# Kernel optimization log

Measured on AMD Instinct MI355X. Metric: run time of the kernel, lower is better.

The kernel has to match this reference:

```python
import jax, jax.numpy as jnp
import numpy as np
from jax.nn import gelu

L = 4        # N_layers
M = 32       # N_modes
PA = 48      # n_processor_a
PB = 48      # n_processor_b
P = PA + PB
IN_A, IN_B = 3, 3
OUT_A, OUT_B = 1, 1
HA, HB = 256, 128
K = 3        # kernel_size
S3 = 0.05


def setup_inputs() -> dict:
    key = jax.random.key(0)
    ks = jax.random.split(key, 24)
    n = lambda k, shp, s=1.0: jax.random.normal(k, shp, dtype=jnp.float32) * s
    w_sc = 0.1
    inp = {
        "u_a": n(ks[0], (1, HA, HA)),
        "x_a": n(ks[1], (2, HA, HA)),
        "u_b": n(ks[2], (1, HB, HB)),
        "x_b": n(ks[3], (2, HB, HB)),
        # 1x1 convs stored as (Cout, Cin) matrices (equinox stores (Cout,Cin,1,1); same math)
        "enc_a_w": n(ks[4], (PA, IN_A), w_sc), "enc_a_b": n(ks[5], (PA,), w_sc),
        "enc_b_w": n(ks[6], (PB, IN_B), w_sc), "enc_b_b": n(ks[7], (PB,), w_sc),
        "dec_a_w": n(ks[8], (OUT_A, PA), w_sc), "dec_a_b": n(ks[9], (OUT_A,), w_sc),
        "dec_b_w": n(ks[10], (OUT_B, PB), w_sc), "dec_b_b": n(ks[11], (OUT_B,), w_sc),
        "c1a_w": n(ks[12], (L, PA, PA), w_sc), "c1a_b": n(ks[13], (L, PA), w_sc),
        "c2a_w": n(ks[14], (L, PA, PA), w_sc), "c2a_b": n(ks[15], (L, PA), w_sc),
        "c1b_w": n(ks[16], (L, PB, PB, K, K), w_sc), "c1b_b": n(ks[17], (L, PB), w_sc),
        "c2b_w": n(ks[18], (L, PB, PB, K, K), w_sc), "c2b_b": n(ks[19], (L, PB), w_sc),
        # complex spectral weights A as real/imag float32 parts
        "A_re": n(ks[20], (L, P, P, M, M), S3),
        "A_im": n(ks[21], (L, P, P, M, M), S3),
    }
    return inp


def _conv1x1(x, w, b):
    # x: (Cin, H, W), w: (Cout, Cin)
    return jnp.einsum("oi,ihw->ohw", w, x) + b[:, None, None]


def _convk(x, w, b):
    # x: (Cin, H, W), w: (Cout, Cin, K, K), SAME padding (padding = K//2)
    y = jax.lax.conv_general_dilated(x[None], w, (1, 1), "SAME",
                                     dimension_numbers=("NCHW", "OIHW", "NCHW"))[0]
    return y + b[:, None, None]


def _rfft2_truncate(x, m):
    c = jnp.fft.rfft2(x, norm="forward")[:, :, :m]
    return jnp.roll(c, m // 2, axis=1)[:, :m]


def _irfft2_pad(c, m, s):
    c = jnp.pad(c, ((0, 0), (0, s[0] - c.shape[1]), (0, s[1] - c.shape[2])))
    c = jnp.roll(c, -m // 2, axis=1)
    return jnp.fft.irfft2(c, s=s, norm="forward")


def _spectral(ua, ub, W):
    m = W.shape[2]
    coeff = jnp.concatenate([_rfft2_truncate(ua, m), _rfft2_truncate(ub, m)], axis=0)  # (P, m, m)
    coeff = jnp.einsum("pqmn,qmn->pmn", W, coeff)
    oa = _irfft2_pad(coeff[: ua.shape[0]], m, ua.shape[1:])
    ob = _irfft2_pad(coeff[ua.shape[0]:], m, ub.shape[1:])
    return oa, ob


def reference(u_a, x_a, u_b, x_b,
              enc_a_w, enc_a_b, enc_b_w, enc_b_b,
              dec_a_w, dec_a_b, dec_b_w, dec_b_b,
              c1a_w, c1a_b, c2a_w, c2a_b,
              c1b_w, c1b_b, c2b_w, c2b_b,
              A_re, A_im):
    ua = _conv1x1(jnp.concatenate([x_a, u_a], 0), enc_a_w, enc_a_b)
    ub = _conv1x1(jnp.concatenate([x_b, u_b], 0), enc_b_w, enc_b_b)
    for i in range(A_re.shape[0]):
        Wi = (A_re[i] + 1j * A_im[i]).astype(jnp.complex64)
        ua_, ub_ = _spectral(ua, ub, Wi)
        ua = ua + gelu(_conv1x1(gelu(_conv1x1(ua_, c1a_w[i], c1a_b[i])), c2a_w[i], c2a_b[i]))
        ub = ub + gelu(_convk(gelu(_convk(ub_, c1b_w[i], c1b_b[i])), c2b_w[i], c2b_b[i]))
    out_a = _conv1x1(ua, dec_a_w, dec_a_b)
    out_b = _conv1x1(ub, dec_b_w, dec_b_b)
    return (out_a, out_b)
```

## Files before the change

kernel.cpp:

```cpp
#include <hip/hip_runtime.h>

#define HA 256
#define WA 256
#define HB 128
#define WB 128
#define PA 48
#define PB 48
#define PP 96
#define MM 32
#define NPIXA (HA*WA)
#define NPIXB (HB*WB)

typedef short bf16x8 __attribute__((ext_vector_type(8)));
typedef float f32x4 __attribute__((ext_vector_type(4)));

__device__ __forceinline__ float gelu_f(float x) {
    float z = 0.7978845608028654f * (x + 0.044715f * x * x * x);
    float e = __expf(2.0f * z);
    return x - x / (e + 1.0f);
}

__device__ __forceinline__ short f2bf(float f) {
    unsigned u = __float_as_uint(f);
    unsigned r = (u + 0x7FFFu + ((u >> 16) & 1u)) >> 16;
    return (short)r;
}

__device__ __forceinline__ unsigned pack2(float a, float b) {
    return (unsigned)(unsigned short)f2bf(a) | ((unsigned)(unsigned short)f2bf(b) << 16);
}

__global__ __launch_bounds__(256) void k_pre(
        float* tiyA, float* tixB, float* tiyB, short* T2x,
        const float* u_a, const float* x_a, const float* u_b, const float* x_b,
        const float* wa, const float* ba, const float* wb, const float* bb,
        float* UA, float* UB,
        const float* c1b_w, const float* c2b_w, short* WT,
        short* TbfA, short* TbfB,
        const float* c1a_w, const float* c2a_w, short* WcT,
        short* Ty2A, short* Ty2B,
        short* TyIA, short* TyIB, short* T2xB) {
    const float TWO_PI = 6.28318530717958647692f;
    int bid = blockIdx.x;
    if (bid < 48) {
        int t = bid * 256 + threadIdx.x;
        if (t < MM * WA) {
            int k = t / WA, x = t - k * WA;
            int m = (k * x) & (WA - 1);
            float ang = TWO_PI * (float)m / (float)WA;
            float s, c; __sincosf(ang, &s, &c);
            float wgt = (k == 0) ? 1.0f : 2.0f;
            T2x[x*64 + 2*k]   = f2bf(wgt * c);
            T2x[x*64 + 2*k+1] = f2bf(-wgt * s);
            int ky = k - 16;
            int my = (ky * x) & (HA - 1);
            float angy = TWO_PI * (float)my / (float)HA;
            float sy, cy; __sincosf(angy, &sy, &cy);
            tiyA[2*t] = cy; tiyA[2*t+1] = sy;
        } else if (t < MM * WA + MM * WB) {
            int t2 = t - MM * WA;
            int k = t2 / WB, x = t2 - k * WB;
            int m = (k * x) & (WB - 1);
            float ang = TWO_PI * (float)m / (float)WB;
            float s, c; __sincosf(ang, &s, &c);
            float wgt = (k == 0) ? 1.0f : 2.0f;
            tixB[2*t2] = wgt * c; tixB[2*t2+1] = wgt * s;
            int ky = k - 16;
            int my = (ky * x) & (HB - 1);
            float angy = TWO_PI * (float)my / (float)HB;
            float sy, cy; __sincosf(angy, &sy, &cy);
            tiyB[2*t2] = cy; tiyB[2*t2+1] = sy;
        }
    } else if (bid < 15408) {
        int eb = bid - 48;
        int o = eb / 320;
        int chunk = eb - o * 320;
        if (chunk < 256) {
            int pix = chunk * 256 + threadIdx.x;
            UA[(size_t)o*NPIXA + pix] = wa[o*3+0]*x_a[pix] + wa[o*3+1]*x_a[NPIXA+pix]
                                      + wa[o*3+2]*u_a[pix] + ba[o];
        } else {
            int pix = (chunk - 256) * 256 + threadIdx.x;
            UB[(size_t)o*NPIXB + pix] = wb[o*3+0]*x_b[pix] + wb[o*3+1]*x_b[NPIXB+pix]
                                      + wb[o*3+2]*u_b[pix] + bb[o];
        }
    } else if (bid < 16272) {
        int g = (bid - 15408) * 256 + threadIdx.x;
        if (g < 4*2*9*48*64) {
            int l  = g / 55296;
            int r1 = g - l*55296;
            int cv = r1 / 27648;
            int r2 = r1 - cv*27648;
            int tap = r2 / 3072;
            int r3 = r2 - tap*3072;
            int oc = r3 >> 6;
            int ic = r3 & 63;
            const float* src = cv ? c2b_w : c1b_w;
            float v = 0.f;
            if (ic < 48) v = src[(((size_t)l*48 + oc)*48 + ic)*9 + tap];
            WT[g] = f2bf(v);
        }
    } else if (bid < 16336) {
        int g = (bid - 16272) * 256 + threadIdx.x;
        int col = g >> 8, x = g & 255;
        int k = col >> 1, comp = col & 1;
        int m = (k * x) & (WA - 1);
        float ang = TWO_PI * (float)m / (float)WA;
        float s, c; __sincosf(ang, &s, &c);
        float sc = 1.0f / (float)(HA * WA);
        TbfA[col*WA + x] = f2bf(comp ? -s * sc : c * sc);
    } else if (bid < 16368) {
        int g = (bid - 16336) * 256 + threadIdx.x;
        int col = g >> 7, x = g & 127;
        int k = col >> 1, comp = col & 1;
        int m = (k * x) & (WB - 1);
        float ang = TWO_PI * (float)m / (float)WB;
        float s, c; __sincosf(ang, &s, &c);
        float sc = 1.0f / (float)(HB * WB);
        TbfB[col*WB + x] = f2bf(comp ? -s * sc : c * sc);
    } else if (bid < 16464) {
        int g = (bid - 16368) * 256 + threadIdx.x;
        int l  = g / 6144;
        int r  = g - l*6144;
        int cv = r / 3072;
        int r2 = r - cv*3072;
        int oc = r2 >> 6;
        int ic = r2 & 63;
        const float* src = cv ? c2a_w : c1a_w;
        float v = 0.f;
        if (ic < 48) v = src[((size_t)l*48 + oc)*48 + ic];
        WcT[g] = f2bf(v);
    } else if (bid < 16592) {
        int g = (bid - 16464) * 256 + threadIdx.x;
        int row = g >> 9, col = g & 511;
        int j = row >> 1, comp = row & 1;
        int y = col >> 1, comp2 = col & 1;
        int my = ((j - 16) * y) & (HA - 1);
        float ang = TWO_PI * (float)my / (float)HA;
        float sy, cy; __sincosf(ang, &sy, &cy);
        float v = comp == 0 ? (comp2 == 0 ? cy : sy) : (comp2 == 0 ? -sy : cy);
        Ty2A[g] = f2bf(v);
    } else if (bid < 16656) {
        int g = (bid - 16592) * 256 + threadIdx.x;
        int row = g >> 8, col = g & 255;
        int j = row >> 1, comp = row & 1;
        int y = col >> 1, comp2 = col & 1;
        int my = ((j - 16) * y) & (HB - 1);
        float ang = TWO_PI * (float)my / (float)HB;
        float sy, cy; __sincosf(ang, &sy, &cy);
        float v = comp == 0 ? (comp2 == 0 ? cy : sy) : (comp2 == 0 ? -sy : cy);
        Ty2B[g] = f2bf(v);
    } else if (bid < 16720) {
        int g = (bid - 16656) * 256 + threadIdx.x;
        int y = g >> 6, col = g & 63;
        int j = col >> 1, comp = col & 1;
        int my = ((j - 16) * y) & (HA - 1);
        float ang = TWO_PI * (float)my / (float)HA;
        float sy, cy; __sincosf(ang, &sy, &cy);
        TyIA[g] = f2bf(comp ? sy : cy);
    } else if (bid < 16752) {
        int g = (bid - 16720) * 256 + threadIdx.x;
        int y = g >> 6, col = g & 63;
        int j = col >> 1, comp = col & 1;
        int my = ((j - 16) * y) & (HB - 1);
        float ang = TWO_PI * (float)my / (float)HB;
        float sy, cy; __sincosf(ang, &sy, &cy);
        TyIB[g] = f2bf(comp ? sy : cy);
    } else {
        int g = (bid - 16752) * 256 + threadIdx.x;
        int x = g >> 6, col = g & 63;
        int k = col >> 1, comp = col & 1;
        int m = (k * x) & (WB - 1);
        float ang = TWO_PI * (float)m / (float)WB;
        float s, c; __sincosf(ang, &s, &c);
        float wgt = (k == 0) ? 1.0f : 2.0f;
        T2xB[g] = f2bf(comp ? -wgt * s : wgt * c);
    }
}

__global__ __launch_bounds__(256) void k_fwd_x(
        const float* __restrict__ UA, const float* __restrict__ UB,
        short* __restrict__ FTA, short* __restrict__ FTB,
        const short* __restrict__ TbfA, const short* __restrict__ TbfB) {
    extern __shared__ short lsb[];
    int bid = blockIdx.x;
    const float* U; short* FT; const short* T; int N, ymask, cshift;
    if (bid < 384) { U = UA; FT = FTA; T = TbfA; N = WA; ymask = 255; cshift = 8; }
    else { bid -= 384; U = UB; FT = FTB; T = TbfB; N = WB; ymask = 127; cshift = 7; }
    int r0 = bid * 32;
    int c = r0 >> cshift;
    int ybase = r0 & ymask;
    int NP = N + 8;
    int nq = N >> 2;
    const float4* src = (const float4*)(U + (size_t)r0 * N);
    for (int i = threadIdx.x; i < 32*nq; i += 256) {
        int r = i / nq, q = i - r*nq;
        float4 v = src[i];
        *(uint2*)(lsb + r*NP + q*4) = make_uint2(pack2(v.x, v.y), pack2(v.z, v.w));
    }
    __syncthreads();
    int wv = threadIdx.x >> 6, lane = threadIdx.x & 63;
    int n = lane & 15, kg = lane >> 4;
    int col = wv*16 + n;
    const short* Tc = T + (size_t)col * N;
    f32x4 acc0 = {0.f,0.f,0.f,0.f}, acc1 = {0.f,0.f,0.f,0.f};
    for (int ks = 0; ks < (N >> 5); ++ks) {
        bf16x8 bfrag = *(const bf16x8*)(Tc + ks*32 + kg*8);
        bf16x8 a0 = *(const bf16x8*)(lsb + (size_t)n*NP + ks*32 + kg*8);
        bf16x8 a1 = *(const bf16x8*)(lsb + (size_t)(16+n)*NP + ks*32 + kg*8);
        acc0 = __builtin_amdgcn_mfma_f32_16x16x32_bf16(a0, bfrag, acc0, 0, 0, 0);
        acc1 = __builtin_amdgcn_mfma_f32_16x16x32_bf16(a1, bfrag, acc1, 0, 0, 0);
    }
    __syncthreads();
    short* trb = lsb;
    #pragma unroll
    for (int r = 0; r < 4; ++r) {
        trb[col*36 + kg*4 + r]      = f2bf(acc0[r]);
        trb[col*36 + 16 + kg*4 + r] = f2bf(acc1[r]);
    }
    __syncthreads();
    int K2 = 2 * (ymask + 1);
    for (int idx = threadIdx.x; idx < 512; idx += 256) {
        int kx = idx >> 4, q = idx & 15;
        int yl = q * 2;
        unsigned lo = (unsigned)(unsigned short)trb[(2*kx+0)*36 + yl]
                    | ((unsigned)(unsigned short)trb[(2*kx+1)*36 + yl] << 16);
        unsigned hi = (unsigned)(unsigned short)trb[(2*kx+0)*36 + yl+1]
                    | ((unsigned)(unsigned short)trb[(2*kx+1)*36 + yl+1] << 16);
        *(uint2*)(FT + ((size_t)(c*32 + kx))*K2 + 2*(size_t)ybase + yl*2) = make_uint2(lo, hi);
    }
}

__global__ __launch_bounds__(256) void k_fwd_y(
        const short* __restrict__ FTA, const short* __restrict__ FTB,
        const short* __restrict__ Ty2A, const short* __restrict__ Ty2B,
        float* __restrict__ CINa, float* __restrict__ CINb) {
    __shared__ short lsb[32*264];
    int bid = blockIdx.x;
    const short* FT; const short* Ty; int K2, NP, pbase, c, h;
    if (bid < 96) { c = bid>>1; h = bid&1; FT = FTA; Ty = Ty2A; K2 = 512; NP = 264; pbase = 0; }
    else { int b2 = bid - 96; c = b2>>1; h = b2&1; FT = FTB; Ty = Ty2B; K2 = 256; NP = 136; pbase = 48; }
    float* CO = (h == 0) ? CINa : CINb;
    int hlen = K2 >> 1;
    int nchunk = hlen >> 3;
    for (int idx = threadIdx.x; idx < 32*nchunk; idx += 256) {
        int row = idx / nchunk, q = idx - row*nchunk;
        *(uint4*)(lsb + row*NP + q*8) =
            *(const uint4*)(FT + ((size_t)c*32 + row)*K2 + h*hlen + q*8);
    }
    __syncthreads();
    int w = threadIdx.x >> 6, lane = threadIdx.x & 63;
    int n = lane & 15, kg = lane >> 4;
    f32x4 acc0 = {0.f,0.f,0.f,0.f}, acc1 = {0.f,0.f,0.f,0.f};
    int nks = hlen >> 5;
    for (int ks = 0; ks < nks; ++ks) {
        bf16x8 af = *(const bf16x8*)(Ty + (size_t)(w*16 + n)*K2 + h*hlen + ks*32 + kg*8);
        bf16x8 b0 = *(const bf16x8*)(lsb + n*NP + ks*32 + kg*8);
        bf16x8 b1 = *(const bf16x8*)(lsb + (16+n)*NP + ks*32 + kg*8);
        acc0 = __builtin_amdgcn_mfma_f32_16x16x32_bf16(af, b0, acc0, 0, 0, 0);
        acc1 = __builtin_amdgcn_mfma_f32_16x16x32_bf16(af, b1, acc1, 0, 0, 0);
    }
    #pragma unroll
    for (int r = 0; r < 4; ++r) {
        int row = w*16 + kg*4 + r;
        int j = row >> 1, comp = row & 1;
        size_t base = (((size_t)(pbase + c))*32 + j)*32;
        CO[(base + n)*2 + comp]      = acc0[r];
        CO[(base + 16 + n)*2 + comp] = acc1[r];
    }
}

__global__ __launch_bounds__(256) void k_spectral(
        const float* __restrict__ Wre, const float* __restrict__ Wim,
        const float* __restrict__ CINa, const float* __restrict__ CINb,
        float2* __restrict__ PART) {
    int part = blockIdx.y;
    int t = blockIdx.x * 256 + threadIdx.x;
    int p = t >> 8;
    int m4 = (t & 255) << 2;
    int q0 = part * 12;
    const float4* wr = (const float4*)(Wre + ((size_t)p * PP + q0) * 1024 + m4);
    const float4* wi = (const float4*)(Wim + ((size_t)p * PP + q0) * 1024 + m4);
    const float4* ca = (const float4*)(CINa + (size_t)q0 * 2048 + m4*2);
    const float4* cb = (const float4*)(CINb + (size_t)q0 * 2048 + m4*2);
    float re0=0,re1=0,re2=0,re3=0, im0=0,im1=0,im2=0,im3=0;
    #pragma unroll
    for (int q = 0; q < 12; ++q) {
        float4 a = wr[q * 256];
        float4 b = wi[q * 256];
        float4 c0 = ca[q * 512];
        float4 c1 = ca[q * 512 + 1];
        float4 d0 = cb[q * 512];
        float4 d1 = cb[q * 512 + 1];
        float cr0 = c0.x + d0.x, ci0 = c0.y + d0.y;
        float cr1 = c0.z + d0.z, ci1 = c0.w + d0.w;
        float cr2 = c1.x + d1.x, ci2 = c1.y + d1.y;
        float cr3 = c1.z + d1.z, ci3 = c1.w + d1.w;
        re0 += a.x*cr0 - b.x*ci0;  im0 += a.x*ci0 + b.x*cr0;
        re1 += a.y*cr1 - b.y*ci1;  im1 += a.y*ci1 + b.y*cr1;
        re2 += a.z*cr2 - b.z*ci2;  im2 += a.z*ci2 + b.z*cr2;
        re3 += a.w*cr3 - b.w*ci3;  im3 += a.w*ci3 + b.w*cr3;
    }
    float2* po = PART + ((size_t)part * PP + p) * 1024 + m4;
    po[0] = make_float2(re0, im0);
    po[1] = make_float2(re1, im1);
    po[2] = make_float2(re2, im2);
    po[3] = make_float2(re3, im3);
}

__global__ __launch_bounds__(256) void k_invy(
        const float2* __restrict__ PART,
        const short* __restrict__ TyIA, const short* __restrict__ TyIB,
        short* __restrict__ DA, short* __restrict__ DB) {
    __shared__ short A2[64*72];
    int bid = blockIdx.x;
    int c, yh, cb; const short* Ty; short* D;
    if (bid < 96) { c = bid >> 1; yh = bid & 1; Ty = TyIA; D = DA; cb = c; }
    else { c = bid - 96 + 48; yh = 0; Ty = TyIB; D = DB; cb = c - 48; }
    for (int idx = threadIdx.x; idx < 1024; idx += 256) {
        int j = idx >> 5, kx = idx & 31;
        float re = 0.f, im = 0.f;
        const float2* pp = PART + (size_t)c*1024 + idx;
        #pragma unroll
        for (int u = 0; u < 8; ++u) {
            float2 v = pp[(size_t)u*PP*1024];
            re += v.x; im += v.y;
        }
        A2[(2*kx+0)*72 + 2*j]   = f2bf(re);
        A2[(2*kx+0)*72 + 2*j+1] = f2bf(-im);
        A2[(2*kx+1)*72 + 2*j]   = f2bf(im);
        A2[(2*kx+1)*72 + 2*j+1] = f2bf(re);
    }
    __syncthreads();
    int wv = threadIdx.x >> 6, lane = threadIdx.x & 63;
    int n = lane & 15, kg = lane >> 4;
    #pragma unroll
    for (int ntl = 0; ntl < 2; ++ntl) {
        int nt = wv*2 + ntl;
        int y = yh*128 + nt*16 + n;
        bf16x8 bf0 = *(const bf16x8*)(Ty + (size_t)y*64 + kg*8);
        bf16x8 bf1 = *(const bf16x8*)(Ty + (size_t)y*64 + 32 + kg*8);
        #pragma unroll
        for (int mt = 0; mt < 4; ++mt) {
            bf16x8 a0 = *(const bf16x8*)(A2 + (mt*16 + n)*72 + kg*8);
            bf16x8 a1 = *(const bf16x8*)(A2 + (mt*16 + n)*72 + 32 + kg*8);
            f32x4 acc = {0.f,0.f,0.f,0.f};
            acc = __builtin_amdgcn_mfma_f32_16x16x32_bf16(a0, bf0, acc, 0, 0, 0);
            acc = __builtin_amdgcn_mfma_f32_16x16x32_bf16(a1, bf1, acc, 0, 0, 0);
            int row0 = mt*16 + kg*4;
            *(uint2*)(D + (size_t)y*3072 + cb*64 + row0) =
                make_uint2(pack2(acc[0], acc[1]), pack2(acc[2], acc[3]));
        }
    }
}

__global__ __launch_bounds__(256) void k_inv(
        const short* __restrict__ DA, const short* __restrict__ DB,
        float* __restrict__ UA, short* __restrict__ SBbf,
        const short* __restrict__ T2x, const short* __restrict__ T2xB,
        const short* __restrict__ W1T, const short* __restrict__ W2T,
        const float* __restrict__ b1v, const float* __restrict__ b2v) {
    __shared__ __attribute__((aligned(16))) char smc[37888];
    int t = threadIdx.x;
    int wv = t >> 6, lane = t & 63;
    int n = lane & 15, kg = lane >> 4;
    if (blockIdx.x < 512) {
        short* b0bf  = (short*)smc;
        short* slbf  = (short*)(smc + 18432);
        float* bl1   = (float*)(smc + 37120);
        float* bl2   = (float*)(smc + 37312);
        int y  = blockIdx.x >> 1;
        int xh = (blockIdx.x & 1) << 7;
        if (t >= 64 && t < 112) bl1[t-64] = b1v[t-64];
        if (t >= 128 && t < 176) bl2[t-128] = b2v[t-128];
        const short* DAy = DA + (size_t)y*3072;
        {
            f32x4 acc[2][3];
            #pragma unroll
            for (int i = 0; i < 2; ++i)
                #pragma unroll
                for (int mt = 0; mt < 3; ++mt)
                    acc[i][mt] = (f32x4){0.f,0.f,0.f,0.f};
            #pragma unroll
            for (int ks = 0; ks < 2; ++ks) {
                bf16x8 bfr[2];
                #pragma unroll
                for (int i = 0; i < 2; ++i) {
                    int px = xh + (wv*2 + i)*16 + n;
                    bfr[i] = *(const bf16x8*)(T2x + (size_t)px*64 + ks*32 + kg*8);
                }
                #pragma unroll
                for (int mt = 0; mt < 3; ++mt) {
                    bf16x8 af = *(const bf16x8*)(DAy + (mt*16 + n)*64 + ks*32 + kg*8);
                    #pragma unroll
                    for (int i = 0; i < 2; ++i)
                        acc[i][mt] = __builtin_amdgcn_mfma_f32_16x16x32_bf16(af, bfr[i], acc[i][mt], 0, 0, 0);
                }
            }
            #pragma unroll
            for (int i = 0; i < 2; ++i) {
                int xl = (wv*2 + i)*16 + n;
                #pragma unroll
                for (int mt = 0; mt < 3; ++mt)
                    #pragma unroll
                    for (int r = 0; r < 4; ++r)
                        slbf[xl*72 + mt*16 + kg*4 + r] = f2bf(acc[i][mt][r]);
            }
            for (int idx = t; idx < 2048; idx += 256)
                slbf[(idx >> 4)*72 + 48 + (idx & 15)] = 0;
        }
        __syncthreads();
        {
            bf16x8 aw[3][2];
            #pragma unroll
            for (int mt = 0; mt < 3; ++mt)
                #pragma unroll
                for (int ks = 0; ks < 2; ++ks)
                    aw[mt][ks] = *(const bf16x8*)(W1T + (size_t)(mt*16 + n)*64 + ks*32 + kg*8);
            f32x4 acc[2][3];
            #pragma unroll
            for (int nt = 0; nt < 2; ++nt)
                #pragma unroll
                for (int mt = 0; mt < 3; ++mt)
                    acc[nt][mt] = (f32x4){0.f,0.f,0.f,0.f};
            #pragma unroll
            for (int nt = 0; nt < 2; ++nt) {
                int ntile = wv*2 + nt;
                #pragma unroll
                for (int ks = 0; ks < 2; ++ks) {
                    bf16x8 bfrag = *(const bf16x8*)(slbf + (size_t)(ntile*16 + n)*72 + ks*32 + kg*8);
                    #pragma unroll
                    for (int mt = 0; mt < 3; ++mt)
                        acc[nt][mt] = __builtin_amdgcn_mfma_f32_16x16x32_bf16(aw[mt][ks], bfrag, acc[nt][mt], 0, 0, 0);
                }
            }
            #pragma unroll
            for (int nt = 0; nt < 2; ++nt) {
                int px = (wv*2 + nt)*16 + n;
                #pragma unroll
                for (int mt = 0; mt < 3; ++mt) {
                    int oc0 = mt*16 + kg*4;
                    float g0 = gelu_f(acc[nt][mt][0] + bl1[oc0+0]);
                    float g1 = gelu_f(acc[nt][mt][1] + bl1[oc0+1]);
                    float g2 = gelu_f(acc[nt][mt][2] + bl1[oc0+2]);
                    float g3 = gelu_f(acc[nt][mt][3] + bl1[oc0+3]);
                    *(uint2*)(b0bf + (size_t)px*72 + oc0) = make_uint2(pack2(g0,g1), pack2(g2,g3));
                }
            }
            for (int idx = t; idx < 2048; idx += 256)
                b0bf[(idx >> 4)*72 + 48 + (idx & 15)] = 0;
        }
        __syncthreads();
        {
            bf16x8 aw[3][2];
            #pragma unroll
            for (int mt = 0; mt < 3; ++mt)
                #pragma unroll
                for (int ks = 0; ks < 2; ++ks)
                    aw[mt][ks] = *(const bf16x8*)(W2T + (size_t)(mt*16 + n)*64 + ks*32 + kg*8);
            f32x4 acc[2][3];
            #pragma unroll
            for (int nt = 0; nt < 2; ++nt)
                #pragma unroll
                for (int mt = 0; mt < 3; ++mt)
                    acc[nt][mt] = (f32x4){0.f,0.f,0.f,0.f};
            #pragma unroll
            for (int nt = 0; nt < 2; ++nt) {
                int ntile = wv*2 + nt;
                #pragma unroll
                for (int ks = 0; ks < 2; ++ks) {
                    bf16x8 bfrag = *(const bf16x8*)(b0bf + (size_t)(ntile*16 + n)*72 + ks*32 + kg*8);
                    #pragma unroll
                    for (int mt = 0; mt < 3; ++mt)
                        acc[nt][mt] = __builtin_amdgcn_mfma_f32_16x16x32_bf16(aw[mt][ks], bfrag, acc[nt][mt], 0, 0, 0);
                }
            }
            #pragma unroll
            for (int nt = 0; nt < 2; ++nt) {
                int px = (wv*2 + nt)*16 + n;
                #pragma unroll
                for (int mt = 0; mt < 3; ++mt) {
                    int oc0 = mt*16 + kg*4;
                    #pragma unroll
                    for (int r = 0; r < 4; ++r) {
                        int oc = oc0 + r;
                        size_t o = (size_t)oc*NPIXA + (size_t)y*WA + xh + px;
                        UA[o] = gelu_f(acc[nt][mt][r] + bl2[oc]) + UA[o];
                    }
                }
            }
        }
    } else {
        int y = blockIdx.x - 512;
        short* sbuf = (short*)smc;
        const short* DBy = DB + (size_t)y*3072;
        #pragma unroll
        for (int ntl = 0; ntl < 2; ++ntl) {
            int nt = wv*2 + ntl;
            int x = nt*16 + n;
            bf16x8 bf0 = *(const bf16x8*)(T2xB + (size_t)x*64 + kg*8);
            bf16x8 bf1 = *(const bf16x8*)(T2xB + (size_t)x*64 + 32 + kg*8);
            #pragma unroll
            for (int mt = 0; mt < 3; ++mt) {
                bf16x8 a0 = *(const bf16x8*)(DBy + (mt*16 + n)*64 + kg*8);
                bf16x8 a1 = *(const bf16x8*)(DBy + (mt*16 + n)*64 + 32 + kg*8);
                f32x4 acc = {0.f,0.f,0.f,0.f};
                acc = __builtin_amdgcn_mfma_f32_16x16x32_bf16(a0, bf0, acc, 0, 0, 0);
                acc = __builtin_amdgcn_mfma_f32_16x16x32_bf16(a1, bf1, acc, 0, 0, 0);
                int c0 = mt*16 + kg*4;
                #pragma unroll
                for (int r = 0; r < 4; ++r)
                    sbuf[(c0 + r)*132 + x] = f2bf(acc[r]);
            }
        }
        __syncthreads();
        for (int idx = t; idx < 3072; idx += 256) {
            int x = idx / 24, cu = idx - x*24;
            unsigned v = (unsigned)(unsigned short)sbuf[(2*cu)*132 + x]
                       | ((unsigned)(unsigned short)sbuf[(2*cu+1)*132 + x] << 16);
            *(unsigned*)(SBbf + ((size_t)y*WB + x)*48 + 2*cu) = v;
        }
    }
}

__global__ __launch_bounds__(384) void k_conv3x3_mfma(
        const short* __restrict__ in, float* __restrict__ outf,
        short* __restrict__ outbf,
        const short* __restrict__ wt, const float* __restrict__ bias,
        const float* resid) {
    __shared__ __attribute__((aligned(16))) short tile[3*34*72];
    int y  = blockIdx.x >> 2;
    int x0 = (blockIdx.x & 3) << 5;
    int tid = threadIdx.x;
    for (int idx = tid; idx < 102*6; idx += 384) {
        int pix = idx / 6, chunk = idx - pix*6;
        int r = pix / 34, px = pix - r*34;
        int gy = y - 1 + r, gx = x0 - 1 + px;
        uint4 v = {0u,0u,0u,0u};
        if (gy >= 0 && gy < HB && gx >= 0 && gx < WB)
            v = *(const uint4*)(in + ((size_t)gy*WB + gx)*48 + chunk*8);
        *(uint4*)(tile + pix*72 + chunk*8) = v;
    }
    for (int idx = tid; idx < 102*2; idx += 384) {
        int pix = idx >> 1, h = idx & 1;
        *(uint4*)(tile + pix*72 + 48 + h*8) = (uint4){0u,0u,0u,0u};
    }
    __syncthreads();

    int wv = tid / 64, lane = tid & 63;
    int n = lane & 15, kg = lane >> 4;
    int nt = wv & 1, mt = wv >> 1;
    f32x4 acc = {0.f,0.f,0.f,0.f};
    #pragma unroll
    for (int tap = 0; tap < 9; ++tap) {
        int dy = tap / 3, dx = tap - dy*3;
        int pxl = nt*16 + n + dx;
        const short* brow = tile + (dy*34 + pxl)*72;
        const short* ap = wt + (size_t)tap*3072 + (size_t)(mt*16 + n)*64;
        #pragma unroll
        for (int ks = 0; ks < 2; ++ks) {
            bf16x8 bfrag = *(const bf16x8*)(brow + ks*32 + kg*8);
            bf16x8 afrag = *(const bf16x8*)(ap + ks*32 + kg*8);
            acc = __builtin_amdgcn_mfma_f32_16x16x32_bf16(afrag, bfrag, acc, 0, 0, 0);
        }
    }
    int px_g = x0 + nt*16 + n;
    int oc0 = mt*16 + kg*4;
    float g0 = gelu_f(acc[0] + bias[oc0+0]);
    float g1 = gelu_f(acc[1] + bias[oc0+1]);
    float g2 = gelu_f(acc[2] + bias[oc0+2]);
    float g3 = gelu_f(acc[3] + bias[oc0+3]);
    if (outbf) {
        *(uint2*)(outbf + ((size_t)y*WB + px_g)*48 + oc0) =
            make_uint2(pack2(g0, g1), pack2(g2, g3));
    } else {
        float gv[4] = {g0, g1, g2, g3};
        #pragma unroll
        for (int r = 0; r < 4; ++r) {
            size_t o = (size_t)(oc0 + r)*NPIXB + (size_t)y*WB + px_g;
            outf[o] = gv[r] + resid[o];
        }
    }
}

__global__ __launch_bounds__(256) void k_decode(
        const float* __restrict__ UA, const float* __restrict__ UB,
        const float* dwa, const float* dba,
        const float* dwb, const float* dbb, float* outp) {
    int t = blockIdx.x*256 + threadIdx.x;
    if (t < NPIXA) {
        float acc = dba[0];
        #pragma unroll 8
        for (int p = 0; p < PA; ++p) acc += dwa[p]*UA[(size_t)p*NPIXA + t];
        outp[t] = acc;
    } else {
        int u = t - NPIXA;
        float acc = dbb[0];
        #pragma unroll 8
        for (int p = 0; p < PB; ++p) acc += dwb[p]*UB[(size_t)p*NPIXB + u];
        outp[t] = acc;
    }
}

extern "C" void kernel_launch(void* const* d_in, const int* in_sizes, int n_in,
                              void* d_out, int out_size, void* d_ws, size_t ws_size,
                              hipStream_t stream) {
    const float* u_a   = (const float*)d_in[0];
    const float* x_a   = (const float*)d_in[1];
    const float* u_b   = (const float*)d_in[2];
    const float* x_b   = (const float*)d_in[3];
    const float* enc_a_w = (const float*)d_in[4];
    const float* enc_a_b = (const float*)d_in[5];
    const float* enc_b_w = (const float*)d_in[6];
    const float* enc_b_b = (const float*)d_in[7];
    const float* dec_a_w = (const float*)d_in[8];
    const float* dec_a_b = (const float*)d_in[9];
    const float* dec_b_w = (const float*)d_in[10];
    const float* dec_b_b = (const float*)d_in[11];
    const float* c1a_w = (const float*)d_in[12];
    const float* c1a_b = (const float*)d_in[13];
    const float* c2a_w = (const float*)d_in[14];
    const float* c2a_b = (const float*)d_in[15];
    const float* c1b_w = (const float*)d_in[16];
    const float* c1b_b = (const float*)d_in[17];
    const float* c2b_w = (const float*)d_in[18];
    const float* c2b_b = (const float*)d_in[19];
    const float* A_re = (const float*)d_in[20];
    const float* A_im = (const float*)d_in[21];

    float* ws = (float*)d_ws;
    size_t off = 0;
    auto alloc = [&](size_t n) { float* p = ws + off; off += n; return p; };
    short* WT    = (short*)alloc(4*2*9*48*64/2);
    short* TbfA  = (short*)alloc(64*WA/2);
    short* TbfB  = (short*)alloc(64*WB/2);
    short* WcT   = (short*)alloc(4*2*48*64/2);
    short* T2x   = (short*)alloc(WA*64/2);
    short* T2xB  = (short*)alloc(WB*64/2);
    short* Ty2A  = (short*)alloc(64*512/2);
    short* Ty2B  = (short*)alloc(64*256/2);
    short* TyIA  = (short*)alloc(HA*64/2);
    short* TyIB  = (short*)alloc(HB*64/2);
    float* TiyA  = alloc(MM*HA*2);
    float* TixB  = alloc(MM*WB*2);
    float* TiyB  = alloc(MM*HB*2);
    float* UA = alloc((size_t)PA*NPIXA);
    float* UB = alloc((size_t)PB*NPIXB);
    short* SBbf = (short*)alloc((size_t)PB*NPIXB/2);
    short* TBbf = (short*)alloc((size_t)PB*NPIXB/2);
    short* FTA = (short*)alloc((size_t)PA*MM*512/2);
    short* FTB = (short*)alloc((size_t)PB*MM*256/2);
    short* DA  = (short*)alloc((size_t)HA*3072/2);
    short* DB  = (short*)alloc((size_t)HB*3072/2);
    float* CINa = alloc((size_t)PP*MM*MM*2);
    float* CINb = alloc((size_t)PP*MM*MM*2);
    float2* PART = (float2*)alloc((size_t)8*PP*MM*MM*2);
    if (off * sizeof(float) > ws_size) return;

    k_pre<<<dim3(16784), dim3(256), 0, stream>>>(
        TiyA, TixB, TiyB, T2x,
        u_a,x_a,u_b,x_b, enc_a_w,enc_a_b,enc_b_w,enc_b_b, UA,UB,
        c1b_w, c2b_w, WT, TbfA, TbfB, c1a_w, c2a_w, WcT, Ty2A, Ty2B,
        TyIA, TyIB, T2xB);
    for (int l = 0; l < 4; ++l) {
        k_fwd_x<<<dim3(576), dim3(256), 32*(WA+8)*2, stream>>>(UA,UB,FTA,FTB,TbfA,TbfB);
        k_fwd_y<<<dim3(192), dim3(256), 0, stream>>>(FTA,FTB,Ty2A,Ty2B,CINa,CINb);
        k_spectral<<<dim3(96,8), dim3(256), 0, stream>>>(
            A_re + (size_t)l*PP*PP*MM*MM, A_im + (size_t)l*PP*PP*MM*MM,
            CINa, CINb, PART);
        k_invy<<<dim3(144), dim3(256), 0, stream>>>(PART, TyIA, TyIB, DA, DB);
        k_inv<<<dim3(512 + 128), dim3(256), 0, stream>>>(DA, DB, UA, SBbf,
            T2x, T2xB,
            WcT + (size_t)(l*2 + 0)*3072, WcT + (size_t)(l*2 + 1)*3072,
            c1a_b + (size_t)l*PA, c2a_b + (size_t)l*PA);
        k_conv3x3_mfma<<<dim3(512), dim3(384), 0, stream>>>(SBbf, (float*)nullptr, TBbf,
            WT + (size_t)(l*2 + 0)*27648, c1b_b + (size_t)l*PB, (const float*)nullptr);
        k_conv3x3_mfma<<<dim3(512), dim3(384), 0, stream>>>(TBbf, UB, (short*)nullptr,
            WT + (size_t)(l*2 + 1)*27648, c2b_b + (size_t)l*PB, UB);
    }
    k_decode<<<dim3(320), dim3(256), 0, stream>>>(UA, UB,
        dec_a_w, dec_a_b, dec_b_w, dec_b_b, (float*)d_out);
}
```

Baseline: 308.0 us.

## Split fwd_y K into quarters with reduction kernel; double invy and conv3x3 grids

The forward y-DFT kernel now splits its reduction dimension four ways instead of two, writing four partial coefficient buffers. A new small kernel sums them once, so the spectral kernel reads a single pre-summed input instead of adding two buffers in every block. The inverse-y kernel and the 3x3 convolution are also split into smaller blocks (twice as many, each doing half the work) to raise parallelism across CUs. The cost is one extra kernel launch per layer, more partial-sum traffic, and more halo reloads in the narrower conv tiles.

```diff
diff --git a/kernel.cpp b/kernel.cpp
--- a/kernel.cpp
+++ b/kernel.cpp
@@ -234,14 +234,14 @@
 __global__ __launch_bounds__(256) void k_fwd_y(
         const short* __restrict__ FTA, const short* __restrict__ FTB,
         const short* __restrict__ Ty2A, const short* __restrict__ Ty2B,
-        float* __restrict__ CINa, float* __restrict__ CINb) {
-    __shared__ short lsb[32*264];
+        float* __restrict__ CIN4) {
+    __shared__ short lsb[32*136];
     int bid = blockIdx.x;
     const short* FT; const short* Ty; int K2, NP, pbase, c, h;
-    if (bid < 96) { c = bid>>1; h = bid&1; FT = FTA; Ty = Ty2A; K2 = 512; NP = 264; pbase = 0; }
-    else { int b2 = bid - 96; c = b2>>1; h = b2&1; FT = FTB; Ty = Ty2B; K2 = 256; NP = 136; pbase = 48; }
-    float* CO = (h == 0) ? CINa : CINb;
-    int hlen = K2 >> 1;
+    if (bid < 192) { c = bid>>2; h = bid&3; FT = FTA; Ty = Ty2A; K2 = 512; NP = 136; pbase = 0; }
+    else { int b2 = bid - 192; c = b2>>2; h = b2&3; FT = FTB; Ty = Ty2B; K2 = 256; NP = 72; pbase = 48; }
+    float* CO = CIN4 + (size_t)h * (PP*MM*MM*2);
+    int hlen = K2 >> 2;
     int nchunk = hlen >> 3;
     for (int idx = threadIdx.x; idx < 32*nchunk; idx += 256) {
         int row = idx / nchunk, q = idx - row*nchunk;
@@ -270,10 +270,18 @@
     }
 }
 
+__global__ __launch_bounds__(256) void k_csum(
+        const float4* __restrict__ CIN4, float4* __restrict__ CINs) {
+    int t = blockIdx.x * 256 + threadIdx.x;
+    const int S = PP*MM*MM*2/4;
+    float4 a = CIN4[t], b = CIN4[t + S], c = CIN4[t + 2*S], d = CIN4[t + 3*S];
+    CINs[t] = make_float4(a.x+b.x+c.x+d.x, a.y+b.y+c.y+d.y,
+                          a.z+b.z+c.z+d.z, a.w+b.w+c.w+d.w);
+}
+
 __global__ __launch_bounds__(256) void k_spectral(
         const float* __restrict__ Wre, const float* __restrict__ Wim,
-        const float* __restrict__ CINa, const float* __restrict__ CINb,
-        float2* __restrict__ PART) {
+        const float* __restrict__ CINs, float2* __restrict__ PART) {
     int part = blockIdx.y;
     int t = blockIdx.x * 256 + threadIdx.x;
     int p = t >> 8;
@@ -281,8 +289,7 @@
     int q0 = part * 12;
     const float4* wr = (const float4*)(Wre + ((size_t)p * PP + q0) * 1024 + m4);
     const float4* wi = (const float4*)(Wim + ((size_t)p * PP + q0) * 1024 + m4);
-    const float4* ca = (const float4*)(CINa + (size_t)q0 * 2048 + m4*2);
-    const float4* cb = (const float4*)(CINb + (size_t)q0 * 2048 + m4*2);
+    const float4* ca = (const float4*)(CINs + (size_t)q0 * 2048 + m4*2);
     float re0=0,re1=0,re2=0,re3=0, im0=0,im1=0,im2=0,im3=0;
     #pragma unroll
     for (int q = 0; q < 12; ++q) {
@@ -290,16 +297,10 @@
         float4 b = wi[q * 256];
         float4 c0 = ca[q * 512];
         float4 c1 = ca[q * 512 + 1];
-        float4 d0 = cb[q * 512];
-        float4 d1 = cb[q * 512 + 1];
-        float cr0 = c0.x + d0.x, ci0 = c0.y + d0.y;
-        float cr1 = c0.z + d0.z, ci1 = c0.w + d0.w;
-        float cr2 = c1.x + d1.x, ci2 = c1.y + d1.y;
-        float cr3 = c1.z + d1.z, ci3 = c1.w + d1.w;
-        re0 += a.x*cr0 - b.x*ci0;  im0 += a.x*ci0 + b.x*cr0;
-        re1 += a.y*cr1 - b.y*ci1;  im1 += a.y*ci1 + b.y*cr1;
-        re2 += a.z*cr2 - b.z*ci2;  im2 += a.z*ci2 + b.z*cr2;
-        re3 += a.w*cr3 - b.w*ci3;  im3 += a.w*ci3 + b.w*cr3;
+        re0 += a.x*c0.x - b.x*c0.y;  im0 += a.x*c0.y + b.x*c0.x;
+        re1 += a.y*c0.z - b.y*c0.w;  im1 += a.y*c0.w + b.y*c0.z;
+        re2 += a.z*c1.x - b.z*c1.y;  im2 += a.z*c1.y + b.z*c1.x;
+        re3 += a.w*c1.z - b.w*c1.w;  im3 += a.w*c1.w + b.w*c1.z;
     }
     float2* po = PART + ((size_t)part * PP + p) * 1024 + m4;
     po[0] = make_float2(re0, im0);
@@ -314,9 +315,9 @@
         short* __restrict__ DA, short* __restrict__ DB) {
     __shared__ short A2[64*72];
     int bid = blockIdx.x;
-    int c, yh, cb; const short* Ty; short* D;
-    if (bid < 96) { c = bid >> 1; yh = bid & 1; Ty = TyIA; D = DA; cb = c; }
-    else { c = bid - 96 + 48; yh = 0; Ty = TyIB; D = DB; cb = c - 48; }
+    int c, ybase, cb; const short* Ty; short* D;
+    if (bid < 192) { c = bid >> 2; ybase = (bid & 3) * 64; Ty = TyIA; D = DA; cb = c; }
+    else { int b2 = bid - 192; c = 48 + (b2 >> 1); ybase = (b2 & 1) * 64; Ty = TyIB; D = DB; cb = c - 48; }
     for (int idx = threadIdx.x; idx < 1024; idx += 256) {
         int j = idx >> 5, kx = idx & 31;
         float re = 0.f, im = 0.f;
@@ -334,23 +335,19 @@
     __syncthreads();
     int wv = threadIdx.x >> 6, lane = threadIdx.x & 63;
     int n = lane & 15, kg = lane >> 4;
+    int y = ybase + wv*16 + n;
+    bf16x8 bf0 = *(const bf16x8*)(Ty + (size_t)y*64 + kg*8);
+    bf16x8 bf1 = *(const bf16x8*)(Ty + (size_t)y*64 + 32 + kg*8);
     #pragma unroll
-    for (int ntl = 0; ntl < 2; ++ntl) {
-        int nt = wv*2 + ntl;
-        int y = yh*128 + nt*16 + n;
-        bf16x8 bf0 = *(const bf16x8*)(Ty + (size_t)y*64 + kg*8);
-        bf16x8 bf1 = *(const bf16x8*)(Ty + (size_t)y*64 + 32 + kg*8);
-        #pragma unroll
-        for (int mt = 0; mt < 4; ++mt) {
-            bf16x8 a0 = *(const bf16x8*)(A2 + (mt*16 + n)*72 + kg*8);
-            bf16x8 a1 = *(const bf16x8*)(A2 + (mt*16 + n)*72 + 32 + kg*8);
-            f32x4 acc = {0.f,0.f,0.f,0.f};
-            acc = __builtin_amdgcn_mfma_f32_16x16x32_bf16(a0, bf0, acc, 0, 0, 0);
-            acc = __builtin_amdgcn_mfma_f32_16x16x32_bf16(a1, bf1, acc, 0, 0, 0);
-            int row0 = mt*16 + kg*4;
-            *(uint2*)(D + (size_t)y*3072 + cb*64 + row0) =
-                make_uint2(pack2(acc[0], acc[1]), pack2(acc[2], acc[3]));
-        }
+    for (int mt = 0; mt < 4; ++mt) {
+        bf16x8 a0 = *(const bf16x8*)(A2 + (mt*16 + n)*72 + kg*8);
+        bf16x8 a1 = *(const bf16x8*)(A2 + (mt*16 + n)*72 + 32 + kg*8);
+        f32x4 acc = {0.f,0.f,0.f,0.f};
+        acc = __builtin_amdgcn_mfma_f32_16x16x32_bf16(a0, bf0, acc, 0, 0, 0);
+        acc = __builtin_amdgcn_mfma_f32_16x16x32_bf16(a1, bf1, acc, 0, 0, 0);
+        int row0 = mt*16 + kg*4;
+        *(uint2*)(D + (size_t)y*3072 + cb*64 + row0) =
+            make_uint2(pack2(acc[0], acc[1]), pack2(acc[2], acc[3]));
     }
 }
 
@@ -523,39 +520,37 @@
     }
 }
 
-__global__ __launch_bounds__(384) void k_conv3x3_mfma(
+__global__ __launch_bounds__(192) void k_conv3x3_mfma(
         const short* __restrict__ in, float* __restrict__ outf,
         short* __restrict__ outbf,
         const short* __restrict__ wt, const float* __restrict__ bias,
         const float* resid) {
-    __shared__ __attribute__((aligned(16))) short tile[3*34*72];
-    int y  = blockIdx.x >> 2;
-    int x0 = (blockIdx.x & 3) << 5;
+    __shared__ __attribute__((aligned(16))) short tile[3*18*72];
+    int y  = blockIdx.x >> 3;
+    int x0 = (blockIdx.x & 7) << 4;
     int tid = threadIdx.x;
-    for (int idx = tid; idx < 102*6; idx += 384) {
+    for (int idx = tid; idx < 54*6; idx += 192) {
         int pix = idx / 6, chunk = idx - pix*6;
-        int r = pix / 34, px = pix - r*34;
+        int r = pix / 18, px = pix - r*18;
         int gy = y - 1 + r, gx = x0 - 1 + px;
         uint4 v = {0u,0u,0u,0u};
         if (gy >= 0 && gy < HB && gx >= 0 && gx < WB)
             v = *(const uint4*)(in + ((size_t)gy*WB + gx)*48 + chunk*8);
         *(uint4*)(tile + pix*72 + chunk*8) = v;
     }
-    for (int idx = tid; idx < 102*2; idx += 384) {
+    for (int idx = tid; idx < 54*2; idx += 192) {
         int pix = idx >> 1, h = idx & 1;
         *(uint4*)(tile + pix*72 + 48 + h*8) = (uint4){0u,0u,0u,0u};
     }
     __syncthreads();
 
-    int wv = tid / 64, lane = tid & 63;
+    int mt = tid / 64, lane = tid & 63;
     int n = lane & 15, kg = lane >> 4;
-    int nt = wv & 1, mt = wv >> 1;
     f32x4 acc = {0.f,0.f,0.f,0.f};
     #pragma unroll
     for (int tap = 0; tap < 9; ++tap) {
         int dy = tap / 3, dx = tap - dy*3;
-        int pxl = nt*16 + n + dx;
-        const short* brow = tile + (dy*34 + pxl)*72;
+        const short* brow = tile + (dy*18 + n + dx)*72;
         const short* ap = wt + (size_t)tap*3072 + (size_t)(mt*16 + n)*64;
         #pragma unroll
         for (int ks = 0; ks < 2; ++ks) {
@@ -564,7 +559,7 @@
             acc = __builtin_amdgcn_mfma_f32_16x16x32_bf16(afrag, bfrag, acc, 0, 0, 0);
         }
     }
-    int px_g = x0 + nt*16 + n;
+    int px_g = x0 + n;
     int oc0 = mt*16 + kg*4;
     float g0 = gelu_f(acc[0] + bias[oc0+0]);
     float g1 = gelu_f(acc[1] + bias[oc0+1]);
@@ -652,8 +647,8 @@
     short* FTB = (short*)alloc((size_t)PB*MM*256/2);
     short* DA  = (short*)alloc((size_t)HA*3072/2);
     short* DB  = (short*)alloc((size_t)HB*3072/2);
-    float* CINa = alloc((size_t)PP*MM*MM*2);
-    float* CINb = alloc((size_t)PP*MM*MM*2);
+    float* CIN4 = alloc((size_t)4*PP*MM*MM*2);
+    float* CINs = alloc((size_t)PP*MM*MM*2);
     float2* PART = (float2*)alloc((size_t)8*PP*MM*MM*2);
     if (off * sizeof(float) > ws_size) return;
 
@@ -664,18 +659,19 @@
         TyIA, TyIB, T2xB);
     for (int l = 0; l < 4; ++l) {
         k_fwd_x<<<dim3(576), dim3(256), 32*(WA+8)*2, stream>>>(UA,UB,FTA,FTB,TbfA,TbfB);
-        k_fwd_y<<<dim3(192), dim3(256), 0, stream>>>(FTA,FTB,Ty2A,Ty2B,CINa,CINb);
+        k_fwd_y<<<dim3(384), dim3(256), 0, stream>>>(FTA,FTB,Ty2A,Ty2B,CIN4);
+        k_csum<<<dim3(192), dim3(256), 0, stream>>>((const float4*)CIN4, (float4*)CINs);
         k_spectral<<<dim3(96,8), dim3(256), 0, stream>>>(
             A_re + (size_t)l*PP*PP*MM*MM, A_im + (size_t)l*PP*PP*MM*MM,
-            CINa, CINb, PART);
-        k_invy<<<dim3(144), dim3(256), 0, stream>>>(PART, TyIA, TyIB, DA, DB);
+            CINs, PART);
+        k_invy<<<dim3(288), dim3(256), 0, stream>>>(PART, TyIA, TyIB, DA, DB);
         k_inv<<<dim3(512 + 128), dim3(256), 0, stream>>>(DA, DB, UA, SBbf,
             T2x, T2xB,
             WcT + (size_t)(l*2 + 0)*3072, WcT + (size_t)(l*2 + 1)*3072,
             c1a_b + (size_t)l*PA, c2a_b + (size_t)l*PA);
-        k_conv3x3_mfma<<<dim3(512), dim3(384), 0, stream>>>(SBbf, (float*)nullptr, TBbf,
+        k_conv3x3_mfma<<<dim3(1024), dim3(192), 0, stream>>>(SBbf, (float*)nullptr, TBbf,
             WT + (size_t)(l*2 + 0)*27648, c1b_b + (size_t)l*PB, (const float*)nullptr);
-        k_conv3x3_mfma<<<dim3(512), dim3(384), 0, stream>>>(TBbf, UB, (short*)nullptr,
+        k_conv3x3_mfma<<<dim3(1024), dim3(192), 0, stream>>>(TBbf, UB, (short*)nullptr,
             WT + (size_t)(l*2 + 1)*27648, c2b_b + (size_t)l*PB, UB);
     }
     k_decode<<<dim3(320), dim3(256), 0, stream>>>(UA, UB,
```

Result: slower. 317.0 us (+2.9%).
